# Performance work log

Measured on AMD Instinct MI355X. Metric: run time of the kernel, lower is better.

The kernel has to match this reference:

```python
import jax, jax.numpy as jnp
import numpy as np

NUM_ROUNDS = 2
NUM_REVERSE_ROUNDS = 2


def _scatter_mean(x, src, dst, n):
    # PyG mean aggregation: out[i] = mean_{(src->i) in E} x[src]; 0 if no in-edges.
    deg = jax.ops.segment_sum(jnp.ones((src.shape[0],), x.dtype), dst, num_segments=n)
    s = jax.ops.segment_sum(x[src], dst, num_segments=n)
    return s / jnp.maximum(deg, 1.0)[:, None]


def setup_inputs() -> dict:
    key = jax.random.key(0)
    ks = jax.random.split(key, 12)
    N_TEXT, N_NON, E, EMB, R = 100000, 10000, 500000, 256, 500
    N = N_TEXT + N_NON
    PRED_IN = 4 * EMB + 2 * 2 + 2 * 2 * (NUM_ROUNDS + NUM_REVERSE_ROUNDS)  # 1044
    return {
        "h_id_tensor": jax.random.randint(ks[0], (E,), 0, N),
        "r_id_tensor": jax.random.randint(ks[1], (E,), 0, R),
        "t_id_tensor": jax.random.randint(ks[2], (E,), 0, N),
        "q_emb": jax.random.normal(ks[3], (EMB,), jnp.float32),
        "entity_embs": jax.random.normal(ks[4], (N_TEXT, EMB), jnp.float32),
        "num_non_text_entities": N_NON,
        "relation_embs": jax.random.normal(ks[5], (R, EMB), jnp.float32),
        "topic_entity_one_hot": jax.random.uniform(ks[6], (N, 2), jnp.float32),
        "non_text_emb": jax.random.normal(ks[7], (1, EMB), jnp.float32),
        "W1": jax.random.normal(ks[8], (PRED_IN, EMB), jnp.float32) * 0.02,
        "b1": jnp.zeros((EMB,), jnp.float32),
        "W2": jax.random.normal(ks[9], (EMB, 1), jnp.float32) * 0.02,
        "b2": jnp.zeros((1,), jnp.float32),
    }


def reference(h_id_tensor, r_id_tensor, t_id_tensor, q_emb, entity_embs,
              num_non_text_entities, relation_embs, topic_entity_one_hot,
              non_text_emb, W1, b1, W2, b2):
    n = entity_embs.shape[0] + num_non_text_entities
    # h_e base: text entity embs + broadcast non-text embedding
    h_e0 = jnp.concatenate(
        [entity_embs, jnp.broadcast_to(non_text_emb, (num_non_text_entities, non_text_emb.shape[1]))],
        axis=0)
    h_e_list = [h_e0, topic_entity_one_hot]
    # DDE forward rounds: messages flow h_id -> t_id
    h_pe = topic_entity_one_hot
    for _ in range(NUM_ROUNDS):
        h_pe = _scatter_mean(h_pe, h_id_tensor, t_id_tensor, n)
        h_e_list.append(h_pe)
    # reverse rounds: messages flow t_id -> h_id
    h_pe = topic_entity_one_hot
    for _ in range(NUM_REVERSE_ROUNDS):
        h_pe = _scatter_mean(h_pe, t_id_tensor, h_id_tensor, n)
        h_e_list.append(h_pe)
    h_e = jnp.concatenate(h_e_list, axis=1)  # [N, emb + 2 + 2*(R+Rr)]
    e = h_id_tensor.shape[0]
    h_triple = jnp.concatenate(
        [jnp.broadcast_to(q_emb[None, :], (e, q_emb.shape[0])),
         h_e[h_id_tensor],
         relation_embs[r_id_tensor],
         h_e[t_id_tensor]], axis=1)  # [E, 1044]
    hidden = jax.nn.relu(h_triple @ W1 + b1)
    return hidden @ W2 + b2
```

## Files before the change

### kernel.cpp

```cpp
#include <hip/hip_runtime.h>
#include <stdint.h>

#define EMB 256
#define LDKB 288
#define DDE 10

typedef __attribute__((ext_vector_type(8))) short short8;
typedef __attribute__((ext_vector_type(4))) float f32x4;

__device__ __forceinline__ unsigned short f2bf(float f) {
    union { float f; unsigned int u; } v; v.f = f;
    unsigned int u = v.u;
    unsigned int r = (u + 0x7FFFu + ((u >> 16) & 1u)) >> 16;
    return (unsigned short)r;
}
__device__ __forceinline__ float bf2f(unsigned short b) {
    union { unsigned int u; float f; } v; v.u = ((unsigned int)b) << 16;
    return v.f;
}

#define FPSCALE 1048576.0f
#define FPINV   (1.0f / 1048576.0f)

__device__ __forceinline__ unsigned long long pack2(float a, float b) {
    unsigned int ua = (unsigned int)(a * FPSCALE);
    unsigned int ub = (unsigned int)(b * FPSCALE);
    return ((unsigned long long)ua << 36) | ((unsigned long long)ub << 10);
}
__device__ __forceinline__ float2 unpack2(unsigned long long v) {
    float d = fmaxf((float)(unsigned int)(v & 0x3FFULL), 1.0f);
    return make_float2((float)((v >> 36) & 0x3FFFFFFULL) * FPINV / d,
                       (float)((v >> 10) & 0x3FFFFFFULL) * FPINV / d);
}
__device__ __forceinline__ float2 unpack2d(unsigned long long v, float d) {
    return make_float2((float)((v >> 36) & 0x3FFFFFFULL) * FPINV / d,
                       (float)((v >> 10) & 0x3FFFFFFULL) * FPINV / d);
}


__global__ void k_r1_fused(const int* __restrict__ h_id, const int* __restrict__ t_id,
                           const float2* __restrict__ topic,
                           unsigned long long* __restrict__ fwd,
                           unsigned long long* __restrict__ rev, int E, int SC1, int COPY, int WT_BLK,
                           int R, int TOTAL,
                           const float4* __restrict__ entity, const float4* __restrict__ nontext,
                           ushort4* __restrict__ he4, int n_text, int N,
                           const float* __restrict__ W1, unsigned short* __restrict__ wT,
                           const float* __restrict__ qv, const float* __restrict__ rel,
                           const float* __restrict__ b1, unsigned short* __restrict__ Prb,
                           float* __restrict__ cw) {
    const int b = blockIdx.x;
    const int sc_before = (int)(((long long)b * SC1) / TOTAL);
    const int is_scatter = (int)(((long long)(b + 1) * SC1) / TOTAL) != sc_before;
    if (is_scatter) {
        int e = sc_before * 256 + threadIdx.x;
        if (e >= E) return;
        int h = h_id[e], t = t_id[e];
        float2 th = topic[h];
        float2 tt = topic[t];
        atomicAdd(&fwd[t], pack2(th.x, th.y) | 1ULL);
        atomicAdd(&rev[h], pack2(tt.x, tt.y) | 1ULL);
        return;
    }
    const int o = b - sc_before;
    if (o < COPY) {
        int idx = o * 256 + threadIdx.x;
        int n = idx >> 6, q = idx & 63;
        float4 v = make_float4(0.f, 0.f, 0.f, 0.f);
        if (n < N) v = (n < n_text) ? entity[(size_t)n * 64 + q] : nontext[q];
        he4[(size_t)n * 64 + q] = make_ushort4(f2bf(v.x), f2bf(v.y), f2bf(v.z), f2bf(v.w));
    } else if (o < COPY + WT_BLK) {
        int idx = (o - COPY) * 256 + threadIdx.x;
        int j = idx / LDKB;
        int k = idx - j * LDKB;
        int col   = (j < EMB) ? j : (j - EMB);
        int baseE = (j < EMB) ? 256 : 778;
        int baseD = (j < EMB) ? 512 : 1034;
        float v = 0.0f;
        if (k < EMB)            v = W1[(long long)(baseE + k) * EMB + col];
        else if (k < EMB + DDE) v = W1[(long long)(baseD + (k - EMB)) * EMB + col];
        wT[idx] = f2bf(v);
    } else if (o < COPY + WT_BLK + R) {
        int r = o - COPY - WT_BLK;
        int j = threadIdx.x;
        float acc = b1[j];
        for (int k = 0; k < EMB; ++k)
            acc = fmaf(qv[k], W1[(long long)k * EMB + j], acc);
        const float* relr = rel + (long long)r * EMB;
        for (int k = 0; k < EMB; ++k)
            acc = fmaf(relr[k], W1[(long long)(522 + k) * EMB + j], acc);
        Prb[(long long)r * EMB + j] = f2bf(acc);
    } else {
        int idx = (o - COPY - WT_BLK - R) * 256 + threadIdx.x;
        if (idx < 2048) {
            int j = idx >> 2, c = idx & 3;
            int col   = (j < EMB) ? j : (j - EMB);
            int baseD = (j < EMB) ? 512 : 1034;
            int row   = baseD + ((c < 2) ? (4 + c) : (8 + (c - 2)));
            cw[idx] = W1[(long long)row * EMB + col];
        }
    }
}

__global__ __launch_bounds__(512) void k_gemm_r2(const unsigned short* __restrict__ he,
                                                 const unsigned short* __restrict__ wT,
                                                 unsigned short* __restrict__ Ph,
                                                 unsigned short* __restrict__ Pt,
                                                 const float2* __restrict__ topic,
                                                 const unsigned long long* __restrict__ fwd,
                                                 const unsigned long long* __restrict__ rev,
                                                 unsigned long long* __restrict__ s2,
                                                 unsigned long long* __restrict__ sr2,
                                                 const int* __restrict__ h_id,
                                                 const int* __restrict__ t_id,
                                                 int N, int E, int GB, int TOTAL) {
    __shared__ __align__(16) unsigned short lA[2][128 * 32];
    __shared__ __align__(16) unsigned short lB[2][256 * 32];
    const int b = blockIdx.x;
    const int g_before = (int)(((long long)b * GB) / TOTAL);
    const int is_gemm = (int)(((long long)(b + 1) * GB) / TOTAL) != g_before;
    if (!is_gemm) {
        int e = (b - g_before) * 512 + threadIdx.x;
        if (e < E) {
            int h = h_id[e], t = t_id[e];
            float2 dh = unpack2(fwd[h]);
            float2 rt = unpack2(rev[t]);
            atomicAdd(&s2[t], pack2(dh.x, dh.y));
            atomicAdd(&sr2[h], pack2(rt.x, rt.y));
        }
        return;
    }
    const int t = threadIdx.x;
    const int lane = t & 63;
    const int w = t >> 6;
    const int o = g_before;
    const int bswz = (o & 7) * (GB >> 3) + (o >> 3);
    const int br = bswz >> 1;
    const int bc = bswz & 1;
    const int wr = w >> 2;
    const int wc = w & 3;

    f32x4 acc[4][4];
#pragma unroll
    for (int r = 0; r < 4; ++r)
#pragma unroll
        for (int c = 0; c < 4; ++c)
            acc[r][c] = (f32x4){0.f, 0.f, 0.f, 0.f};

    const char* baseA = (const char*)he + (size_t)(br * 128) * (EMB * 2);
    const char* baseB = (const char*)wT + (size_t)(bc * 256) * (LDKB * 2);

    const int rowX = t >> 2;
    const int colb = (t & 3) * 16;

    auto stage = [&](int k0, int buf) {
        if (k0 < EMB) {
            const char* srcA = baseA + (size_t)rowX * (EMB * 2) + k0 * 2 + colb;
            __builtin_amdgcn_global_load_lds((const __attribute__((address_space(1))) void*)srcA,
                                             (__attribute__((address_space(3))) void*)((char*)lA[buf] + t * 16), 16, 0, 0);
        } else {
            const int n = br * 128 + rowX;
            short8 hv = (short8){0, 0, 0, 0, 0, 0, 0, 0};
            const int q4 = t & 3;
            if (n < N && q4 == 0) {
                float2 tp = topic[n];
                unsigned long long f = fwd[n];
                unsigned long long r = rev[n];
                float2 d1 = unpack2(f);
                float2 r1 = unpack2(r);
                hv[0] = (short)f2bf(tp.x); hv[1] = (short)f2bf(tp.y);
                hv[2] = (short)f2bf(d1.x); hv[3] = (short)f2bf(d1.y);
                hv[6] = (short)f2bf(r1.x); hv[7] = (short)f2bf(r1.y);
            }
            *(short8*)((char*)lA[buf] + rowX * 64 + q4 * 16) = hv;
        }
        const char* srcB0 = baseB + (size_t)rowX * (LDKB * 2) + k0 * 2 + colb;
        const char* srcB1 = baseB + (size_t)(rowX + 128) * (LDKB * 2) + k0 * 2 + colb;
        __builtin_amdgcn_global_load_lds((const __attribute__((address_space(1))) void*)srcB0,
                                         (__attribute__((address_space(3))) void*)((char*)lB[buf] + t * 16), 16, 0, 0);
        __builtin_amdgcn_global_load_lds((const __attribute__((address_space(1))) void*)srcB1,
                                         (__attribute__((address_space(3))) void*)((char*)lB[buf] + 8192 + t * 16), 16, 0, 0);
    };

    const int NK = LDKB / 32;
    stage(0, 0);
    __syncthreads();

    for (int k = 0; k < NK; ++k) {
        const int cur = k & 1;
        if (k + 1 < NK) stage((k + 1) * 32, cur ^ 1);

        short8 af[4], bfr[4];
#pragma unroll
        for (int r = 0; r < 4; ++r) {
            int arow = wr * 64 + r * 16 + (lane & 15);
            af[r] = *(const short8*)(lA[cur] + arow * 32 + (lane >> 4) * 8);
        }
#pragma unroll
        for (int c = 0; c < 4; ++c) {
            int brow = wc * 64 + c * 16 + (lane & 15);
            bfr[c] = *(const short8*)(lB[cur] + brow * 32 + (lane >> 4) * 8);
        }
#pragma unroll
        for (int r = 0; r < 4; ++r)
#pragma unroll
            for (int c = 0; c < 4; ++c)
                acc[r][c] = __builtin_amdgcn_mfma_f32_16x16x32_bf16(af[r], bfr[c], acc[r][c], 0, 0, 0);

        __syncthreads();
    }

    unsigned short* Pout = bc ? Pt : Ph;
    const int nbase = wc * 64;
    const int mbase = br * 128 + wr * 64 + (lane >> 4) * 4;
#pragma unroll
    for (int r = 0; r < 4; ++r) {
#pragma unroll
        for (int c = 0; c < 4; ++c) {
            int n = nbase + c * 16 + (lane & 15);
#pragma unroll
            for (int i = 0; i < 4; ++i) {
                int m = mbase + r * 16 + i;
                Pout[(size_t)m * EMB + n] = f2bf(acc[r][c][i]);
            }
        }
    }
}

__global__ void k_pack(const unsigned long long* __restrict__ fwd,
                       const unsigned long long* __restrict__ rev,
                       const unsigned long long* __restrict__ s2,
                       const unsigned long long* __restrict__ sr2,
                       ushort4* __restrict__ dr2, int N, int Mpad) {
    int n = blockIdx.x * blockDim.x + threadIdx.x;
    if (n >= Mpad) return;
    ushort4 v = make_ushort4(0, 0, 0, 0);
    if (n < N) {
        float df = fmaxf((float)(unsigned int)(fwd[n] & 0x3FFULL), 1.0f);
        float dr = fmaxf((float)(unsigned int)(rev[n] & 0x3FFULL), 1.0f);
        float2 d2 = unpack2d(s2[n], df);
        float2 r2 = unpack2d(sr2[n], dr);
        v = make_ushort4(f2bf(d2.x), f2bf(d2.y), f2bf(r2.x), f2bf(r2.y));
    }
    dr2[n] = v;
}

__global__ __launch_bounds__(256) void k_edge(
    const int* __restrict__ h_id, const int* __restrict__ r_id, const int* __restrict__ t_id,
    const unsigned short* __restrict__ Ph, const unsigned short* __restrict__ Pt,
    const unsigned short* __restrict__ Prb, const ushort4* __restrict__ dr2,
    const float4* __restrict__ cw, const float* __restrict__ W2,
    const float* __restrict__ b2, float* __restrict__ out, int E) {
    int lane = threadIdx.x & 63;
    int gw = (blockIdx.x * blockDim.x + threadIdx.x) >> 6;
    int nw = (gridDim.x * blockDim.x) >> 6;
    const int lo = 4 * lane;
    float w2c[4];
    *(float4*)w2c = *(const float4*)(W2 + lo);
    float bb = b2[0];
    float4 cH[4], cT[4];
#pragma unroll
    for (int c = 0; c < 4; ++c) { cH[c] = cw[lo + c]; cT[c] = cw[256 + lo + c]; }

    for (int e = gw; e < E; e += nw) {
        int h = h_id[e], r = r_id[e], t = t_id[e];
        ushort4 ph = *(const ushort4*)(Ph + (size_t)h * EMB + lo);
        ushort4 pt = *(const ushort4*)(Pt + (size_t)t * EMB + lo);
        ushort4 pr = *(const ushort4*)(Prb + (size_t)r * EMB + lo);
        ushort4 dh = dr2[h];
        ushort4 dt = dr2[t];
        float d2hx = bf2f(dh.x), d2hy = bf2f(dh.y), r2hx = bf2f(dh.z), r2hy = bf2f(dh.w);
        float d2tx = bf2f(dt.x), d2ty = bf2f(dt.y), r2tx = bf2f(dt.z), r2ty = bf2f(dt.w);
        const unsigned short* phs = (const unsigned short*)&ph;
        const unsigned short* pts = (const unsigned short*)&pt;
        const unsigned short* prs = (const unsigned short*)&pr;
        float acc = 0.f;
#pragma unroll
        for (int c = 0; c < 4; ++c) {
            float v = bf2f(prs[c]) + bf2f(phs[c]) + bf2f(pts[c]);
            v += d2hx * cH[c].x + d2hy * cH[c].y + r2hx * cH[c].z + r2hy * cH[c].w;
            v += d2tx * cT[c].x + d2ty * cT[c].y + r2tx * cT[c].z + r2ty * cT[c].w;
            acc += fmaxf(v, 0.f) * w2c[c];
        }
#pragma unroll
        for (int m = 32; m >= 1; m >>= 1) acc += __shfl_xor(acc, m, 64);
        if (lane == 0) out[e] = acc + bb;
    }
}


extern "C" void kernel_launch(void* const* d_in, const int* in_sizes, int n_in,
                              void* d_out, int out_size, void* d_ws, size_t ws_size,
                              hipStream_t stream) {
    const int*   h_id    = (const int*)d_in[0];
    const int*   r_id    = (const int*)d_in[1];
    const int*   t_id    = (const int*)d_in[2];
    const float* q       = (const float*)d_in[3];
    const float* entity  = (const float*)d_in[4];
    const float* rel     = (const float*)d_in[6];
    const float* topic   = (const float*)d_in[7];
    const float* nontext = (const float*)d_in[8];
    const float* W1      = (const float*)d_in[9];
    const float* b1      = (const float*)d_in[10];
    const float* W2      = (const float*)d_in[11];
    const float* b2      = (const float*)d_in[12];

    const int E      = in_sizes[0];
    const int n_text = in_sizes[4] / EMB;
    const int N      = in_sizes[7] / 2;
    const int R      = in_sizes[6] / EMB;
    const int Mpad   = (N + 127) & ~127;

    char* p = (char*)d_ws;
    auto alloc = [&](size_t bytes) {
        char* r = p;
        p += (bytes + 255) & ~(size_t)255;
        return r;
    };
    unsigned long long* fwd = (unsigned long long*)alloc((size_t)Mpad * 8);
    unsigned long long* rev = (unsigned long long*)alloc((size_t)Mpad * 8);
    unsigned long long* s2  = (unsigned long long*)alloc((size_t)Mpad * 8);
    unsigned long long* sr2 = (unsigned long long*)alloc((size_t)Mpad * 8);
    size_t zero_bytes = (size_t)(p - (char*)d_ws);
    unsigned short* he  = (unsigned short*)alloc((size_t)Mpad * EMB * 2);
    unsigned short* wT  = (unsigned short*)alloc((size_t)512 * LDKB * 2);
    unsigned short* Prb = (unsigned short*)alloc((size_t)R * EMB * 2);
    unsigned short* Ph  = (unsigned short*)alloc((size_t)Mpad * EMB * 2);
    unsigned short* Pt  = (unsigned short*)alloc((size_t)Mpad * EMB * 2);
    ushort4*        dr2 = (ushort4*)alloc((size_t)Mpad * 8);
    float*          cw  = (float*)alloc((size_t)512 * 4 * 4);

    hipMemsetAsync(d_ws, 0, zero_bytes, stream);

    const int T = 256;
    const int SC1 = (E + T - 1) / T;
    const int COPY = Mpad / 4;
    const int WT_BLK = (512 * LDKB) / T;
    const int COEF = 8;
    const int TOTAL1 = SC1 + COPY + WT_BLK + R + COEF;

    k_r1_fused<<<TOTAL1, T, 0, stream>>>(
        h_id, t_id, (const float2*)topic, fwd, rev, E, SC1, COPY, WT_BLK, R, TOTAL1,
        (const float4*)entity, (const float4*)nontext, (ushort4*)he, n_text, N,
        W1, wT, q, rel, b1, Prb, cw);

    const int GB  = (Mpad / 128) * 2;
    const int R2B = (E + 511) / 512;
    k_gemm_r2<<<GB + R2B, 512, 0, stream>>>(he, wT, Ph, Pt,
                                            (const float2*)topic, fwd, rev, s2, sr2,
                                            h_id, t_id, N, E, GB, GB + R2B);

    k_pack<<<(Mpad + T - 1) / T, T, 0, stream>>>(fwd, rev, s2, sr2, dr2, N, Mpad);

    k_edge<<<4096, T, 0, stream>>>(h_id, r_id, t_id, Ph, Pt, Prb, dr2,
                                   (const float4*)cw, W2, b2, (float*)d_out, E);
}
```

Baseline: 294.1 us.

## Fold DDE feature contributions into per-node projections before edge pass

```diff
diff --git a/kernel.cpp b/kernel.cpp
--- a/kernel.cpp
+++ b/kernel.cpp
@@ -6,6 +6,7 @@
 #define DDE 10
 
 typedef __attribute__((ext_vector_type(8))) short short8;
+typedef __attribute__((ext_vector_type(8))) unsigned short ushort8;
 typedef __attribute__((ext_vector_type(4))) float f32x4;
 
 __device__ __forceinline__ unsigned short f2bf(float f) {
@@ -227,61 +228,56 @@
     }
 }
 
-__global__ void k_pack(const unsigned long long* __restrict__ fwd,
-                       const unsigned long long* __restrict__ rev,
-                       const unsigned long long* __restrict__ s2,
-                       const unsigned long long* __restrict__ sr2,
-                       ushort4* __restrict__ dr2, int N, int Mpad) {
-    int n = blockIdx.x * blockDim.x + threadIdx.x;
-    if (n >= Mpad) return;
-    ushort4 v = make_ushort4(0, 0, 0, 0);
-    if (n < N) {
-        float df = fmaxf((float)(unsigned int)(fwd[n] & 0x3FFULL), 1.0f);
-        float dr = fmaxf((float)(unsigned int)(rev[n] & 0x3FFULL), 1.0f);
-        float2 d2 = unpack2d(s2[n], df);
-        float2 r2 = unpack2d(sr2[n], dr);
-        v = make_ushort4(f2bf(d2.x), f2bf(d2.y), f2bf(r2.x), f2bf(r2.y));
-    }
-    dr2[n] = v;
+__global__ __launch_bounds__(256) void k_patch(unsigned short* __restrict__ Ph,
+                                               unsigned short* __restrict__ Pt,
+                                               const unsigned long long* __restrict__ fwd,
+                                               const unsigned long long* __restrict__ rev,
+                                               const unsigned long long* __restrict__ s2,
+                                               const unsigned long long* __restrict__ sr2,
+                                               const float4* __restrict__ cw, int N) {
+    int idx = blockIdx.x * blockDim.x + threadIdx.x;
+    int n = idx >> 6;
+    int g = idx & 63;
+    if (n >= N) return;
+    float df = fmaxf((float)(unsigned int)(fwd[n] & 0x3FFULL), 1.0f);
+    float dr = fmaxf((float)(unsigned int)(rev[n] & 0x3FFULL), 1.0f);
+    float2 d2 = unpack2d(s2[n], df);
+    float2 r2 = unpack2d(sr2[n], dr);
+    unsigned short* P = (g < 32) ? Ph : Pt;
+    const int col = (g & 31) * 8;
+    const int cwb = ((g < 32) ? 0 : 256) + col;
+    ushort8 v = *(const ushort8*)(P + (size_t)n * EMB + col);
+#pragma unroll
+    for (int c = 0; c < 8; ++c) {
+        float4 wv = cw[cwb + c];
+        float x = bf2f((unsigned short)v[c])
+                + d2.x * wv.x + d2.y * wv.y + r2.x * wv.z + r2.y * wv.w;
+        v[c] = f2bf(x);
+    }
+    *(ushort8*)(P + (size_t)n * EMB + col) = v;
 }
 
 __global__ __launch_bounds__(256) void k_edge(
     const int* __restrict__ h_id, const int* __restrict__ r_id, const int* __restrict__ t_id,
     const unsigned short* __restrict__ Ph, const unsigned short* __restrict__ Pt,
-    const unsigned short* __restrict__ Prb, const ushort4* __restrict__ dr2,
-    const float4* __restrict__ cw, const float* __restrict__ W2,
+    const unsigned short* __restrict__ Prb, const float* __restrict__ W2,
     const float* __restrict__ b2, float* __restrict__ out, int E) {
     int lane = threadIdx.x & 63;
     int gw = (blockIdx.x * blockDim.x + threadIdx.x) >> 6;
     int nw = (gridDim.x * blockDim.x) >> 6;
+    float4 w2 = *(const float4*)(W2 + 4 * lane);
+    float bb = b2[0];
     const int lo = 4 * lane;
-    float w2c[4];
-    *(float4*)w2c = *(const float4*)(W2 + lo);
-    float bb = b2[0];
-    float4 cH[4], cT[4];
-#pragma unroll
-    for (int c = 0; c < 4; ++c) { cH[c] = cw[lo + c]; cT[c] = cw[256 + lo + c]; }
-
     for (int e = gw; e < E; e += nw) {
         int h = h_id[e], r = r_id[e], t = t_id[e];
         ushort4 ph = *(const ushort4*)(Ph + (size_t)h * EMB + lo);
         ushort4 pt = *(const ushort4*)(Pt + (size_t)t * EMB + lo);
         ushort4 pr = *(const ushort4*)(Prb + (size_t)r * EMB + lo);
-        ushort4 dh = dr2[h];
-        ushort4 dt = dr2[t];
-        float d2hx = bf2f(dh.x), d2hy = bf2f(dh.y), r2hx = bf2f(dh.z), r2hy = bf2f(dh.w);
-        float d2tx = bf2f(dt.x), d2ty = bf2f(dt.y), r2tx = bf2f(dt.z), r2ty = bf2f(dt.w);
-        const unsigned short* phs = (const unsigned short*)&ph;
-        const unsigned short* pts = (const unsigned short*)&pt;
-        const unsigned short* prs = (const unsigned short*)&pr;
-        float acc = 0.f;
-#pragma unroll
-        for (int c = 0; c < 4; ++c) {
-            float v = bf2f(prs[c]) + bf2f(phs[c]) + bf2f(pts[c]);
-            v += d2hx * cH[c].x + d2hy * cH[c].y + r2hx * cH[c].z + r2hy * cH[c].w;
-            v += d2tx * cT[c].x + d2ty * cT[c].y + r2tx * cT[c].z + r2ty * cT[c].w;
-            acc += fmaxf(v, 0.f) * w2c[c];
-        }
+        float v, acc;
+        v = bf2f(pr.x) + bf2f(ph.x) + bf2f(pt.x); acc  = fmaxf(v, 0.f) * w2.x;
+        v = bf2f(pr.y) + bf2f(ph.y) + bf2f(pt.y); acc += fmaxf(v, 0.f) * w2.y;
+        v = bf2f(pr.z) + bf2f(ph.z) + bf2f(pt.z); acc += fmaxf(v, 0.f) * w2.z;
+        v = bf2f(pr.w) + bf2f(ph.w) + bf2f(pt.w); acc += fmaxf(v, 0.f) * w2.w;
 #pragma unroll
         for (int m = 32; m >= 1; m >>= 1) acc += __shfl_xor(acc, m, 64);
         if (lane == 0) out[e] = acc + bb;
@@ -327,7 +323,6 @@
     unsigned short* Prb = (unsigned short*)alloc((size_t)R * EMB * 2);
     unsigned short* Ph  = (unsigned short*)alloc((size_t)Mpad * EMB * 2);
     unsigned short* Pt  = (unsigned short*)alloc((size_t)Mpad * EMB * 2);
-    ushort4*        dr2 = (ushort4*)alloc((size_t)Mpad * 8);
     float*          cw  = (float*)alloc((size_t)512 * 4 * 4);
 
     hipMemsetAsync(d_ws, 0, zero_bytes, stream);
@@ -350,8 +345,8 @@
                                             (const float2*)topic, fwd, rev, s2, sr2,
                                             h_id, t_id, N, E, GB, GB + R2B);
 
-    k_pack<<<(Mpad + T - 1) / T, T, 0, stream>>>(fwd, rev, s2, sr2, dr2, N, Mpad);
-
-    k_edge<<<4096, T, 0, stream>>>(h_id, r_id, t_id, Ph, Pt, Prb, dr2,
-                                   (const float4*)cw, W2, b2, (float*)d_out, E);
-}
+    k_patch<<<(N * 64 + T - 1) / T, T, 0, stream>>>(Ph, Pt, fwd, rev, s2, sr2,
+                                                    (const float4*)cw, N);
+
+    k_edge<<<4096, T, 0, stream>>>(h_id, r_id, t_id, Ph, Pt, Prb, W2, b2, (float*)d_out, E);
+}
```

Measured after the change: 366.8 us. 1.25x slower.
